# Kernel tuning notes

Measured on AMD Instinct MI355X. Metric: run time of the kernel, lower is better.

Reference implementation:

```python
import jax, jax.numpy as jnp
import numpy as np

B, T, DIM = 2, 1024, 4096
H, Hk, D = 32, 8, 128
NREP = H // Hk
SCALE = 1.0 / np.sqrt(D)
LAMBDA_INIT = 0.8 - 0.6 * np.exp(-0.3 * 0)  # layer_idx=0 -> 0.2
EPS = 1e-6


def setup_inputs() -> dict:
    key = jax.random.key(0)
    ks = jax.random.split(key, 12)
    x = jax.random.normal(ks[0], (B, T, DIM), dtype=jnp.float32)
    cos = jax.random.uniform(ks[1], (T, D // 2), dtype=jnp.float32)
    sin = jax.random.uniform(ks[2], (T, D // 2), dtype=jnp.float32)
    wq = jax.random.normal(ks[3], (DIM, 2 * H * D), dtype=jnp.float32) * 0.02
    wk = jax.random.normal(ks[4], (DIM, 2 * Hk * D), dtype=jnp.float32) * 0.02
    wv = jax.random.normal(ks[5], (DIM, Hk * D), dtype=jnp.float32) * 0.02
    wo = jax.random.normal(ks[6], (H * D, DIM), dtype=jnp.float32) * 0.02
    lambda_q1 = jax.random.normal(ks[7], (H, D), dtype=jnp.float32) * 0.1
    lambda_k1 = jax.random.normal(ks[8], (H, D), dtype=jnp.float32) * 0.1
    lambda_q2 = jax.random.normal(ks[9], (H, D), dtype=jnp.float32) * 0.1
    lambda_k2 = jax.random.normal(ks[10], (H, D), dtype=jnp.float32) * 0.1
    subln_w = jnp.ones((D,), dtype=jnp.float32)
    return {"x": x, "cos": cos, "sin": sin, "wq": wq, "wk": wk, "wv": wv,
            "wo": wo, "lambda_q1": lambda_q1, "lambda_k1": lambda_k1,
            "lambda_q2": lambda_q2, "lambda_k2": lambda_k2, "subln_w": subln_w}


def _rope(xh, cos, sin):
    # xh: [B, h, T, D]; cos/sin: [T, D/2]
    x1, x2 = xh[..., : D // 2], xh[..., D // 2:]
    c = cos[None, None, :, :]
    s = sin[None, None, :, :]
    return jnp.concatenate([x1 * c - x2 * s, x2 * c + x1 * s], axis=-1)


def _causal_attn(q, k, v):
    # q,k,v: [B, H, T, D]
    s = jnp.einsum("bhqd,bhkd->bhqk", q, k) * SCALE
    causal = jnp.tril(jnp.ones((T, T), dtype=bool))
    s = jnp.where(causal[None, None], s, jnp.finfo(s.dtype).min)
    p = jax.nn.softmax(s, axis=-1)
    return jnp.einsum("bhqk,bhkd->bhqd", p, v)


def reference(x, cos, sin, wq, wk, wv, wo, lambda_q1, lambda_k1, lambda_q2, lambda_k2, subln_w):
    q_full = (x @ wq).reshape(B, T, 2 * H, D).transpose(0, 2, 1, 3)   # [B,2H,T,D]
    k_full = (x @ wk).reshape(B, T, 2 * Hk, D).transpose(0, 2, 1, 3)  # [B,2Hk,T,D]
    v = (x @ wv).reshape(B, T, Hk, D).transpose(0, 2, 1, 3)           # [B,Hk,T,D]

    q1, q2 = q_full[:, :H], q_full[:, H:]
    k1, k2 = k_full[:, :Hk], k_full[:, Hk:]

    q1 = _rope(q1, cos, sin)
    q2 = _rope(q2, cos, sin)
    k1 = _rope(k1, cos, sin)
    k2 = _rope(k2, cos, sin)

    def expand_kv(kv):  # [B,Hk,T,D] -> [B,H,T,D] (GQA repeat)
        return jnp.repeat(kv, NREP, axis=1)

    k1e, k2e, ve = expand_kv(k1), expand_kv(k2), expand_kv(v)

    a1 = _causal_attn(q1, k1e, ve)
    a2 = _causal_attn(q2, k2e, ve)

    lam = (jnp.exp(jnp.sum(lambda_q1 * lambda_k1, axis=-1))
           - jnp.exp(jnp.sum(lambda_q2 * lambda_k2, axis=-1))
           + LAMBDA_INIT)  # [H]
    diff = a1 - lam[None, :, None, None] * a2  # [B,H,T,D]

    # per-head-dim RMSNorm (subln)
    rms = jax.lax.rsqrt(jnp.mean(diff * diff, axis=-1, keepdims=True) + EPS)
    diff = diff * rms * subln_w

    out = diff.transpose(0, 2, 1, 3).reshape(B, T, H * D)
    return out @ wo
```

## Files before the change

kernel.cpp:

```cpp
#include <hip/hip_runtime.h>
#include <hip/hip_bf16.h>
#include <stdint.h>

typedef unsigned short u16;
typedef unsigned int u32;
typedef short bf16x8 __attribute__((ext_vector_type(8)));
typedef float f32x4 __attribute__((ext_vector_type(4)));

#define SCALE_F 0.088388347648318447f
#define LAMBDA_INIT_F 0.2f

__device__ __forceinline__ u16 f2bf(float f) {
  union { float f; u32 u; } v; v.f = f;
  u32 r = v.u + 0x7fffu + ((v.u >> 16) & 1u);
  return (u16)(r >> 16);
}
__device__ __forceinline__ float bf2f(u16 u) {
  union { u32 u; float f; } v; v.u = ((u32)u) << 16;
  return v.f;
}

typedef __attribute__((address_space(1))) void gvoid_t;
typedef __attribute__((address_space(3))) void lvoid_t;
__device__ __forceinline__ void gload16(const void* g, void* l) {
  __builtin_amdgcn_global_load_lds((gvoid_t*)g, (lvoid_t*)l, 16, 0, 0);
}

__global__ void cast_f32_bf16(const float4* __restrict__ in, uint2* __restrict__ out, int n4) {
  int i = blockIdx.x * 256 + threadIdx.x;
  if (i >= n4) return;
  float4 v = in[i];
  uint2 o;
  o.x = (u32)f2bf(v.x) | ((u32)f2bf(v.y) << 16);
  o.y = (u32)f2bf(v.z) | ((u32)f2bf(v.w) << 16);
  out[i] = o;
}

__global__ void trans_cast(const float* __restrict__ in, u16* __restrict__ out, int K, int N) {
  __shared__ float tile[64][33];
  int kt = blockIdx.y * 64, nt = blockIdx.x * 32;
  int x = threadIdx.x, y = threadIdx.y;
  #pragma unroll
  for (int j = 0; j < 8; ++j)
    tile[y + j * 8][x] = in[(size_t)(kt + y + j * 8) * N + nt + x];
  __syncthreads();
  #pragma unroll
  for (int j = 0; j < 4; ++j) {
    int n = y * 4 + j;
    u32 pk = (u32)f2bf(tile[2 * x][n]) | ((u32)f2bf(tile[2 * x + 1][n]) << 16);
    *(u32*)&out[(size_t)(nt + n) * K + kt + 2 * x] = pk;
  }
}

#define SQA(buf, t) { \
  gload16(Aq + (size_t)(t) * 32, (buf) + qdst); \
  gload16(Aq + (size_t)64 * K + (size_t)(t) * 32, (buf) + 2048 + qdst); }
#define SQB(buf, t) { \
  gload16(Bq + (size_t)(t) * 32, (buf) + qdst); \
  gload16(Bq + (size_t)64 * K + (size_t)(t) * 32, (buf) + 2048 + qdst); \
  gload16(Bq + (size_t)128 * K + (size_t)(t) * 32, (buf) + 4096 + qdst); \
  gload16(Bq + (size_t)192 * K + (size_t)(t) * 32, (buf) + 6144 + qdst); }
#define QMFMA16(O) { \
  acc[O+0][0] = __builtin_amdgcn_mfma_f32_16x16x32_bf16(a0, b0, acc[O+0][0], 0, 0, 0); \
  acc[O+0][1] = __builtin_amdgcn_mfma_f32_16x16x32_bf16(a0, b1, acc[O+0][1], 0, 0, 0); \
  acc[O+0][2] = __builtin_amdgcn_mfma_f32_16x16x32_bf16(a0, b2, acc[O+0][2], 0, 0, 0); \
  acc[O+0][3] = __builtin_amdgcn_mfma_f32_16x16x32_bf16(a0, b3, acc[O+0][3], 0, 0, 0); \
  acc[O+1][0] = __builtin_amdgcn_mfma_f32_16x16x32_bf16(a1, b0, acc[O+1][0], 0, 0, 0); \
  acc[O+1][1] = __builtin_amdgcn_mfma_f32_16x16x32_bf16(a1, b1, acc[O+1][1], 0, 0, 0); \
  acc[O+1][2] = __builtin_amdgcn_mfma_f32_16x16x32_bf16(a1, b2, acc[O+1][2], 0, 0, 0); \
  acc[O+1][3] = __builtin_amdgcn_mfma_f32_16x16x32_bf16(a1, b3, acc[O+1][3], 0, 0, 0); \
  acc[O+2][0] = __builtin_amdgcn_mfma_f32_16x16x32_bf16(a2, b0, acc[O+2][0], 0, 0, 0); \
  acc[O+2][1] = __builtin_amdgcn_mfma_f32_16x16x32_bf16(a2, b1, acc[O+2][1], 0, 0, 0); \
  acc[O+2][2] = __builtin_amdgcn_mfma_f32_16x16x32_bf16(a2, b2, acc[O+2][2], 0, 0, 0); \
  acc[O+2][3] = __builtin_amdgcn_mfma_f32_16x16x32_bf16(a2, b3, acc[O+2][3], 0, 0, 0); \
  acc[O+3][0] = __builtin_amdgcn_mfma_f32_16x16x32_bf16(a3, b0, acc[O+3][0], 0, 0, 0); \
  acc[O+3][1] = __builtin_amdgcn_mfma_f32_16x16x32_bf16(a3, b1, acc[O+3][1], 0, 0, 0); \
  acc[O+3][2] = __builtin_amdgcn_mfma_f32_16x16x32_bf16(a3, b2, acc[O+3][2], 0, 0, 0); \
  acc[O+3][3] = __builtin_amdgcn_mfma_f32_16x16x32_bf16(a3, b3, acc[O+3][3], 0, 0, 0); }

__global__ __launch_bounds__(256, 2) void gemmW(const u16* __restrict__ A,
                                                const u16* __restrict__ Bt,
                                                u16* __restrict__ C,
                                                int M, int N, int K, int TN) {
  extern __shared__ u16 lds[];
  const int tid = threadIdx.x;
  const int lane = tid & 63;
  const int wn = tid >> 6;
  const int ln = lane & 15, gr = lane >> 4;
  const int NT = K >> 5;

  const int bid = blockIdx.x;
  const int bn = (bid % TN) * 256;
  const int bm = (bid / TN) * 128;

  const int sch = (tid & 3) ^ ((tid >> 3) & 3);
  const u16* Aq = A + (size_t)(bm + (tid >> 2)) * K + sch * 8;
  const u16* Bq = Bt + (size_t)(bn + (tid >> 2)) * K + sch * 8;
  const int qdst = tid * 8;

  const int cfo = (gr ^ ((ln >> 1) & 3)) * 8;
  const int ab = ln * 32 + cfo;
  const int bb = wn * 2048 + ln * 32 + cfo;

  f32x4 acc[8][4] = {};
  bf16x8 a0, a1, a2, a3, b0, b1, b2, b3;

  SQA(lds, 0);
  SQB(lds + 12288, 0);
  SQA(lds + 4096, 1);
  SQB(lds + 20480, 1);
  asm volatile("s_waitcnt vmcnt(6)" ::: "memory");
  __builtin_amdgcn_s_barrier();

  int tm3 = 0;
  for (int t = 0; t < NT; ++t) {
    const u16* Ac = lds + tm3 * 4096;
    const u16* Bc = lds + 12288 + tm3 * 8192;
    int tn3 = tm3 + 2; if (tn3 >= 3) tn3 -= 3;
    u16* An = lds + tn3 * 4096;
    u16* Bn = lds + 12288 + tn3 * 8192;

    a0 = *(const bf16x8*)&Ac[ab];
    a1 = *(const bf16x8*)&Ac[ab + 512];
    a2 = *(const bf16x8*)&Ac[ab + 1024];
    a3 = *(const bf16x8*)&Ac[ab + 1536];
    b0 = *(const bf16x8*)&Bc[bb];
    b1 = *(const bf16x8*)&Bc[bb + 512];
    b2 = *(const bf16x8*)&Bc[bb + 1024];
    b3 = *(const bf16x8*)&Bc[bb + 1536];
    if (t + 2 < NT) SQA(An, t + 2);
    __builtin_amdgcn_s_setprio(1);
    QMFMA16(0);
    __builtin_amdgcn_s_setprio(0);

    a0 = *(const bf16x8*)&Ac[ab + 2048];
    a1 = *(const bf16x8*)&Ac[ab + 2560];
    a2 = *(const bf16x8*)&Ac[ab + 3072];
    a3 = *(const bf16x8*)&Ac[ab + 3584];
    if (t + 2 < NT) {
      SQB(Bn, t + 2);
      asm volatile("s_waitcnt vmcnt(6)" ::: "memory");
    } else {
      asm volatile("s_waitcnt vmcnt(0)" ::: "memory");
    }
    __builtin_amdgcn_s_setprio(1);
    QMFMA16(4);
    __builtin_amdgcn_s_setprio(0);
    __builtin_amdgcn_s_barrier();

    tm3 = (tm3 + 1 == 3) ? 0 : tm3 + 1;
  }

  #pragma unroll
  for (int mf = 0; mf < 8; ++mf) {
    #pragma unroll
    for (int j = 0; j < 4; ++j) {
      int r = bm + mf * 16 + gr * 4 + j;
      #pragma unroll
      for (int nf = 0; nf < 4; ++nf) {
        int c = bn + wn * 64 + nf * 16 + ln;
        C[(size_t)r * N + c] = f2bf(acc[mf][nf][j]);
      }
    }
  }
}

#define STA(buf, t) { \
  gload16(Ab + (size_t)(t) * 64, (buf) + dsloc); \
  gload16(Ab + (size_t)32 * K + (size_t)(t) * 64, (buf) + 2048 + dsloc); \
  gload16(Ab + (size_t)64 * K + (size_t)(t) * 64, (buf) + 4096 + dsloc); \
  gload16(Ab + (size_t)96 * K + (size_t)(t) * 64, (buf) + 6144 + dsloc); }
#define STB(buf, t) { \
  gload16(Bb + (size_t)(t) * 64, (buf) + dsloc); \
  gload16(Bb + (size_t)32 * K + (size_t)(t) * 64, (buf) + 2048 + dsloc); \
  gload16(Bb + (size_t)64 * K + (size_t)(t) * 64, (buf) + 4096 + dsloc); \
  gload16(Bb + (size_t)96 * K + (size_t)(t) * 64, (buf) + 6144 + dsloc); }
#define MFMA16 { \
  acc[0][0] = __builtin_amdgcn_mfma_f32_16x16x32_bf16(a0, b0, acc[0][0], 0, 0, 0); \
  acc[0][1] = __builtin_amdgcn_mfma_f32_16x16x32_bf16(a0, b1, acc[0][1], 0, 0, 0); \
  acc[0][2] = __builtin_amdgcn_mfma_f32_16x16x32_bf16(a0, b2, acc[0][2], 0, 0, 0); \
  acc[0][3] = __builtin_amdgcn_mfma_f32_16x16x32_bf16(a0, b3, acc[0][3], 0, 0, 0); \
  acc[1][0] = __builtin_amdgcn_mfma_f32_16x16x32_bf16(a1, b0, acc[1][0], 0, 0, 0); \
  acc[1][1] = __builtin_amdgcn_mfma_f32_16x16x32_bf16(a1, b1, acc[1][1], 0, 0, 0); \
  acc[1][2] = __builtin_amdgcn_mfma_f32_16x16x32_bf16(a1, b2, acc[1][2], 0, 0, 0); \
  acc[1][3] = __builtin_amdgcn_mfma_f32_16x16x32_bf16(a1, b3, acc[1][3], 0, 0, 0); \
  acc[2][0] = __builtin_amdgcn_mfma_f32_16x16x32_bf16(a2, b0, acc[2][0], 0, 0, 0); \
  acc[2][1] = __builtin_amdgcn_mfma_f32_16x16x32_bf16(a2, b1, acc[2][1], 0, 0, 0); \
  acc[2][2] = __builtin_amdgcn_mfma_f32_16x16x32_bf16(a2, b2, acc[2][2], 0, 0, 0); \
  acc[2][3] = __builtin_amdgcn_mfma_f32_16x16x32_bf16(a2, b3, acc[2][3], 0, 0, 0); \
  acc[3][0] = __builtin_amdgcn_mfma_f32_16x16x32_bf16(a3, b0, acc[3][0], 0, 0, 0); \
  acc[3][1] = __builtin_amdgcn_mfma_f32_16x16x32_bf16(a3, b1, acc[3][1], 0, 0, 0); \
  acc[3][2] = __builtin_amdgcn_mfma_f32_16x16x32_bf16(a3, b2, acc[3][2], 0, 0, 0); \
  acc[3][3] = __builtin_amdgcn_mfma_f32_16x16x32_bf16(a3, b3, acc[3][3], 0, 0, 0); }

template <bool OUT_BF16>
__global__ __launch_bounds__(256, 2) void gemm8p(const u16* __restrict__ A,
                                                 const u16* __restrict__ Bt,
                                                 void* __restrict__ Cv,
                                                 int M, int N, int K, int TN) {
  extern __shared__ u16 lds[];
  const int tid = threadIdx.x;
  const int lane = tid & 63;
  const int wid = tid >> 6;
  const int wm = wid >> 1, wn = wid & 1;
  const int ln = lane & 15, gr = lane >> 4;
  const int NT = K >> 6;

  const int bid = blockIdx.x;
  const int bn = (bid % TN) * 128;
  const int bm = (bid / TN) * 128;

  const int srow = tid >> 3;
  const int sch = (tid & 7) ^ (srow & 7);
  const u16* Ab = A + (size_t)(bm + srow) * K + sch * 8;
  const u16* Bb = Bt + (size_t)(bn + srow) * K + sch * 8;
  const int dsloc = tid * 8;

  const int aro = (wm * 64 + ln) * 64;
  const int bro = (wn * 64 + ln) * 64;
  const int c0 = (gr ^ (ln & 7)) * 8;
  const int c1 = ((4 + gr) ^ (ln & 7)) * 8;

  f32x4 acc[4][4] = {};
  bf16x8 a0, a1, a2, a3, b0, b1, b2, b3;

  STA(lds, 0);
  STB(lds + 16384, 0);
  STB(lds + 24576, 1);
  asm volatile("s_waitcnt vmcnt(4)" ::: "memory");
  __builtin_amdgcn_s_barrier();

  int tm3 = 0;
  for (int t = 0; t < NT; ++t) {
    const u16* Ac = lds + (t & 1) * 8192;
    u16* An = lds + ((t + 1) & 1) * 8192;
    const u16* Bc = lds + 16384 + tm3 * 8192;
    int tn3 = tm3 + 2; if (tn3 >= 3) tn3 -= 3;
    u16* Bn = lds + 16384 + tn3 * 8192;

    a0 = *(const bf16x8*)&Ac[aro + c0];
    a1 = *(const bf16x8*)&Ac[aro + 1024 + c0];
    a2 = *(const bf16x8*)&Ac[aro + 2048 + c0];
    a3 = *(const bf16x8*)&Ac[aro + 3072 + c0];
    b0 = *(const bf16x8*)&Bc[bro + c0];
    b1 = *(const bf16x8*)&Bc[bro + 1024 + c0];
    b2 = *(const bf16x8*)&Bc[bro + 2048 + c0];
    b3 = *(const bf16x8*)&Bc[bro + 3072 + c0];
    if (t + 1 < NT) STA(An, t + 1);
    __builtin_amdgcn_s_setprio(1);
    MFMA16;
    __builtin_amdgcn_s_setprio(0);

    a0 = *(const bf16x8*)&Ac[aro + c1];
    a1 = *(const bf16x8*)&Ac[aro + 1024 + c1];
    a2 = *(const bf16x8*)&Ac[aro + 2048 + c1];
    a3 = *(const bf16x8*)&Ac[aro + 3072 + c1];
    b0 = *(const bf16x8*)&Bc[bro + c1];
    b1 = *(const bf16x8*)&Bc[bro + 1024 + c1];
    b2 = *(const bf16x8*)&Bc[bro + 2048 + c1];
    b3 = *(const bf16x8*)&Bc[bro + 3072 + c1];
    if (t + 2 < NT) {
      STB(Bn, t + 2);
      asm volatile("s_waitcnt vmcnt(4)" ::: "memory");
    } else {
      asm volatile("s_waitcnt vmcnt(0)" ::: "memory");
    }
    __builtin_amdgcn_s_setprio(1);
    MFMA16;
    __builtin_amdgcn_s_setprio(0);
    __builtin_amdgcn_s_barrier();

    tm3 = (tm3 + 1 == 3) ? 0 : tm3 + 1;
  }

  #pragma unroll
  for (int mf = 0; mf < 4; ++mf) {
    #pragma unroll
    for (int j = 0; j < 4; ++j) {
      int r = bm + wm * 64 + mf * 16 + gr * 4 + j;
      #pragma unroll
      for (int nf = 0; nf < 4; ++nf) {
        int c = bn + wn * 64 + nf * 16 + ln;
        if (OUT_BF16) ((u16*)Cv)[(size_t)r * N + c] = f2bf(acc[mf][nf][j]);
        else          ((float*)Cv)[(size_t)r * N + c] = acc[mf][nf][j];
      }
    }
  }
}

__global__ void rope_kernel(const u16* __restrict__ in, u16* __restrict__ out,
                            const float* __restrict__ cosp, const float* __restrict__ sinp,
                            int NHh, int col_off) {
  int idx = blockIdx.x * 256 + threadIdx.x;
  int c = idx & 7;
  int t = (idx >> 3) & 1023;
  int h = (idx >> 13) % NHh;
  int b = (idx >> 13) / NHh;
  size_t src = (size_t)(b * 1024 + t) * 11264 + col_off + h * 128 + c * 8;
  bf16x8 v1 = *(const bf16x8*)&in[src];
  bf16x8 v2 = *(const bf16x8*)&in[src + 64];
  const float4* cp = (const float4*)&cosp[t * 64 + c * 8];
  const float4* sp = (const float4*)&sinp[t * 64 + c * 8];
  float4 c0 = cp[0], c1 = cp[1], s0 = sp[0], s1 = sp[1];
  float cc[8] = {c0.x, c0.y, c0.z, c0.w, c1.x, c1.y, c1.z, c1.w};
  float ss[8] = {s0.x, s0.y, s0.z, s0.w, s1.x, s1.y, s1.z, s1.w};
  bf16x8 o1, o2;
  #pragma unroll
  for (int e = 0; e < 8; ++e) {
    float x1 = bf2f((u16)v1[e]);
    float x2 = bf2f((u16)v2[e]);
    o1[e] = (short)f2bf(x1 * cc[e] - x2 * ss[e]);
    o2[e] = (short)f2bf(x2 * cc[e] + x1 * ss[e]);
  }
  size_t dst = ((size_t)(b * NHh + h) * 1024 + t) * 128 + c * 8;
  *(bf16x8*)&out[dst] = o1;
  *(bf16x8*)&out[dst + 64] = o2;
}

__global__ void vtrans_kernel(const u16* __restrict__ qkv, u16* __restrict__ vt) {
  __shared__ u16 tile[32][34];
  int bh = blockIdx.z;
  int t0 = blockIdx.x * 32, d0 = blockIdx.y * 32;
  int b = bh >> 3, hk = bh & 7;
  int x = threadIdx.x, y = threadIdx.y;
  #pragma unroll
  for (int j = 0; j < 32; j += 8)
    tile[y + j][x] = qkv[(size_t)(b * 1024 + t0 + y + j) * 11264 + 10240 + hk * 128 + d0 + x];
  __syncthreads();
  #pragma unroll
  for (int j = 0; j < 32; j += 8)
    vt[((size_t)bh * 128 + d0 + y + j) * 1024 + t0 + x] = tile[x][y + j];
}

__global__ void lam_kernel(const float* __restrict__ lq1, const float* __restrict__ lk1,
                           const float* __restrict__ lq2, const float* __restrict__ lk2,
                           float* __restrict__ lam) {
  int h = blockIdx.x, l = threadIdx.x;
  float p1 = lq1[h * 128 + l] * lk1[h * 128 + l] + lq1[h * 128 + 64 + l] * lk1[h * 128 + 64 + l];
  float p2 = lq2[h * 128 + l] * lk2[h * 128 + l] + lq2[h * 128 + 64 + l] * lk2[h * 128 + 64 + l];
  #pragma unroll
  for (int m = 32; m >= 1; m >>= 1) { p1 += __shfl_xor(p1, m); p2 += __shfl_xor(p2, m); }
  if (l == 0) lam[h] = expf(p1) - expf(p2) + LAMBDA_INIT_F;
}

__global__ __launch_bounds__(512) void attn_kernel(const u16* __restrict__ qr,
                                                   const u16* __restrict__ kr,
                                                   const u16* __restrict__ vt,
                                                   const float* __restrict__ lam,
                                                   const float* __restrict__ slw,
                                                   u16* __restrict__ attno) {
  __shared__ u16 k1s[2][32 * 136];
  __shared__ u16 k2s[2][32 * 136];
  __shared__ u16 vs[2][128 * 40];
  __shared__ u16 ps[8][2][640];
  const int bx = blockIdx.x, h = blockIdx.y, b = blockIdx.z;
  const int qt = (b == 0) ? (7 - bx) : bx;
  const int tid = threadIdx.x, lane = tid & 63, w = tid >> 6;
  const int ln = lane & 15, gr = lane >> 4;
  const int hk = h >> 2;
  const int qrow0 = qt * 128 + w * 16;
  u16* psw1 = ps[w][0];
  u16* psw2 = ps[w][1];
  const float SL2E = 0.12751744006165926f;
  const float ML2E = 11.541560327111707f;

  bf16x8 q1f[4], q2f[4];
  {
    const u16* q1p = qr + ((size_t)(b * 64 + h) * 1024 + qrow0 + ln) * 128 + gr * 8;
    const u16* q2p = qr + ((size_t)(b * 64 + 32 + h) * 1024 + qrow0 + ln) * 128 + gr * 8;
    #pragma unroll
    for (int ds = 0; ds < 4; ++ds) {
      q1f[ds] = *(const bf16x8*)(q1p + ds * 32);
      q2f[ds] = *(const bf16x8*)(q2p + ds * 32);
    }
  }
  f32x4 acc1[8] = {}, acc2[8] = {};
  float l1[4] = {0.f, 0.f, 0.f, 0.f}, l2[4] = {0.f, 0.f, 0.f, 0.f};

  const u16* k1g = kr + (size_t)(b * 16 + hk) * 1024 * 128;
  const u16* k2g = kr + (size_t)(b * 16 + 8 + hk) * 1024 * 128;
  const u16* vg = vt + (size_t)(b * 8 + hk) * 128 * 1024;
  const int nkt = 4 * qt + 4;

  const int krow = tid >> 4, kch = tid & 15;
  const int vdr = tid >> 2, vch = tid & 3;
  const u16* k1p = k1g + (size_t)krow * 128 + kch * 8;
  const u16* k2p = k2g + (size_t)krow * 128 + kch * 8;
  const u16* vp = vg + (size_t)vdr * 1024 + vch * 8;
  const int kdst = krow * 136 + kch * 8;
  const int vdst = vdr * 40 + vch * 8;

  bf16x8 r0 = *(const bf16x8*)(k1p);
  bf16x8 r1 = *(const bf16x8*)(k2p);
  bf16x8 r2 = *(const bf16x8*)(vp);
  *(bf16x8*)&k1s[0][kdst] = r0;
  *(bf16x8*)&k2s[0][kdst] = r1;
  *(bf16x8*)&vs[0][vdst] = r2;
  __syncthreads();

  int cur = 0;
  for (int kt = 0; kt < nkt; ++kt) {
    if (kt + 1 < nkt) {
      r0 = *(const bf16x8*)(k1p + (size_t)(kt + 1) * 4096);
      r1 = *(const bf16x8*)(k2p + (size_t)(kt + 1) * 4096);
      r2 = *(const bf16x8*)(vp + (size_t)(kt + 1) * 32);
    }

    f32x4 s1[2], s2[2];
    #pragma unroll
    for (int ct = 0; ct < 2; ++ct) {
      s1[ct] = (f32x4){0.f, 0.f, 0.f, 0.f};
      s2[ct] = (f32x4){0.f, 0.f, 0.f, 0.f};
      #pragma unroll
      for (int ds = 0; ds < 4; ++ds) {
        bf16x8 kf1 = *(const bf16x8*)&k1s[cur][(ct * 16 + ln) * 136 + ds * 32 + gr * 8];
        s1[ct] = __builtin_amdgcn_mfma_f32_16x16x32_bf16(q1f[ds], kf1, s1[ct], 0, 0, 0);
        bf16x8 kf2 = *(const bf16x8*)&k2s[cur][(ct * 16 + ln) * 136 + ds * 32 + gr * 8];
        s2[ct] = __builtin_amdgcn_mfma_f32_16x16x32_bf16(q2f[ds], kf2, s2[ct], 0, 0, 0);
      }
    }
    #pragma unroll
    for (int j = 0; j < 4; ++j) {
      int row = qrow0 + gr * 4 + j;
      bool msk0 = (kt * 32 + ln) > row;
      bool msk1 = (kt * 32 + 16 + ln) > row;
      float t10 = msk0 ? -1e30f : fmaf(s1[0][j], SL2E, -ML2E);
      float t11 = msk1 ? -1e30f : fmaf(s1[1][j], SL2E, -ML2E);
      float t20 = msk0 ? -1e30f : fmaf(s2[0][j], SL2E, -ML2E);
      float t21 = msk1 ? -1e30f : fmaf(s2[1][j], SL2E, -ML2E);
      u16 b10 = f2bf(exp2f(t10)), b11 = f2bf(exp2f(t11));
      u16 b20 = f2bf(exp2f(t20)), b21 = f2bf(exp2f(t21));
      int ro = (gr * 4 + j) * 40;
      psw1[ro + ln] = b10; psw1[ro + 16 + ln] = b11;
      psw2[ro + ln] = b20; psw2[ro + 16 + ln] = b21;
      l1[j] += bf2f(b10) + bf2f(b11);
      l2[j] += bf2f(b20) + bf2f(b21);
    }
    bf16x8 pf1 = *(const bf16x8*)&psw1[ln * 40 + gr * 8];
    bf16x8 pf2 = *(const bf16x8*)&psw2[ln * 40 + gr * 8];
    #pragma unroll
    for (int dt = 0; dt < 8; ++dt) {
      bf16x8 vf = *(const bf16x8*)&vs[cur][(dt * 16 + ln) * 40 + gr * 8];
      acc1[dt] = __builtin_amdgcn_mfma_f32_16x16x32_bf16(pf1, vf, acc1[dt], 0, 0, 0);
      acc2[dt] = __builtin_amdgcn_mfma_f32_16x16x32_bf16(pf2, vf, acc2[dt], 0, 0, 0);
    }

    if (kt + 1 < nkt) {
      *(bf16x8*)&k1s[cur ^ 1][kdst] = r0;
      *(bf16x8*)&k2s[cur ^ 1][kdst] = r1;
      *(bf16x8*)&vs[cur ^ 1][vdst] = r2;
    }
    __syncthreads();
    cur ^= 1;
  }

  float inv1[4], inv2[4];
  #pragma unroll
  for (int j = 0; j < 4; ++j) {
    float a = l1[j], c = l2[j];
    a += __shfl_xor(a, 1); a += __shfl_xor(a, 2); a += __shfl_xor(a, 4); a += __shfl_xor(a, 8);
    c += __shfl_xor(c, 1); c += __shfl_xor(c, 2); c += __shfl_xor(c, 4); c += __shfl_xor(c, 8);
    inv1[j] = 1.f / a;
    inv2[j] = 1.f / c;
  }

  float lamv = lam[h];
  float ssq[4] = {0.f, 0.f, 0.f, 0.f};
  #pragma unroll
  for (int dt = 0; dt < 8; ++dt)
    #pragma unroll
    for (int j = 0; j < 4; ++j) {
      float d = acc1[dt][j] * inv1[j] - lamv * (acc2[dt][j] * inv2[j]);
      acc1[dt][j] = d;
      ssq[j] += d * d;
    }
  #pragma unroll
  for (int j = 0; j < 4; ++j) {
    float s = ssq[j];
    s += __shfl_xor(s, 1);
    s += __shfl_xor(s, 2);
    s += __shfl_xor(s, 4);
    s += __shfl_xor(s, 8);
    ssq[j] = rsqrtf(s * (1.0f / 128.0f) + 1e-6f);
  }
  #pragma unroll
  for (int dt = 0; dt < 8; ++dt) {
    float wgt = slw[dt * 16 + ln];
    #pragma unroll
    for (int j = 0; j < 4; ++j) {
      int row = qrow0 + gr * 4 + j;
      attno[(size_t)(b * 1024 + row) * 4096 + h * 128 + dt * 16 + ln] = f2bf(acc1[dt][j] * ssq[j] * wgt);
    }
  }
}

extern "C" void kernel_launch(void* const* d_in, const int* in_sizes, int n_in,
                              void* d_out, int out_size, void* d_ws, size_t ws_size,
                              hipStream_t stream) {
  (void)in_sizes; (void)n_in; (void)out_size; (void)ws_size;
  const float* x    = (const float*)d_in[0];
  const float* cosp = (const float*)d_in[1];
  const float* sinp = (const float*)d_in[2];
  const float* wq   = (const float*)d_in[3];
  const float* wk   = (const float*)d_in[4];
  const float* wv   = (const float*)d_in[5];
  const float* wo   = (const float*)d_in[6];
  const float* lq1  = (const float*)d_in[7];
  const float* lk1  = (const float*)d_in[8];
  const float* lq2  = (const float*)d_in[9];
  const float* lk2  = (const float*)d_in[10];
  const float* slw  = (const float*)d_in[11];
  float* out = (float*)d_out;
  char* ws = (char*)d_ws;

  u16* xb    = (u16*)(ws);
  u16* wqkvt = (u16*)(ws + 16777216);
  u16* qr    = (u16*)(ws + 16777216);
  u16* kr    = (u16*)(ws + 50331648);
  u16* vtp   = (u16*)(ws + 58720256);
  u16* attno = (u16*)(ws + 62914560);
  u16* qkv   = (u16*)(ws + 109051904);
  u16* wot   = (u16*)(ws + 109051904);
  float* lam = (float*)(ws + 155189248);

  cast_f32_bf16<<<8192, 256, 0, stream>>>((const float4*)x, (uint2*)xb, 2097152);
  trans_cast<<<dim3(256, 64), dim3(32, 8), 0, stream>>>(wq, wqkvt, 4096, 8192);
  trans_cast<<<dim3(64, 64),  dim3(32, 8), 0, stream>>>(wk, wqkvt + (size_t)8192 * 4096, 4096, 2048);
  trans_cast<<<dim3(32, 64),  dim3(32, 8), 0, stream>>>(wv, wqkvt + (size_t)10240 * 4096, 4096, 1024);
  gemmW<<<704, 256, 73728, stream>>>(xb, wqkvt, qkv, 2048, 11264, 4096, 44);
  rope_kernel<<<4096, 256, 0, stream>>>(qkv, qr, cosp, sinp, 64, 0);
  rope_kernel<<<1024, 256, 0, stream>>>(qkv, kr, cosp, sinp, 16, 8192);
  vtrans_kernel<<<dim3(32, 4, 16), dim3(32, 8), 0, stream>>>(qkv, vtp);
  trans_cast<<<dim3(128, 64), dim3(32, 8), 0, stream>>>(wo, wot, 4096, 4096);
  lam_kernel<<<32, 64, 0, stream>>>(lq1, lk1, lq2, lk2, lam);
  attn_kernel<<<dim3(8, 32, 2), 512, 0, stream>>>(qr, kr, vtp, lam, slw, attno);
  gemm8p<false><<<512, 256, 81920, stream>>>(attno, wot, (void*)out, 2048, 4096, 4096, 32);
}
```

Measured before the change: 431.3 us.

## Fuse RoPE and head-major scatter into QKV GEMM epilogue

The QKV projection GEMM now stages its output tile in LDS and applies RoPE directly in the epilogue, writing rotated Q and K in head-major layout. V columns go to a compact buffer. This removes the two standalone rope kernels and the round trip of the full QKV intermediate through global memory. In exchange the GEMM epilogue gains an extra LDS pass, a barrier and more complex scattered writes, and the workspace layout is reshuffled.

Result: faster. 419.5 us, median of 2 (-2.8%).

```diff
diff --git a/kernel.cpp b/kernel.cpp
--- a/kernel.cpp
+++ b/kernel.cpp
@@ -80,8 +80,12 @@
 
 __global__ __launch_bounds__(256, 2) void gemmW(const u16* __restrict__ A,
                                                 const u16* __restrict__ Bt,
-                                                u16* __restrict__ C,
-                                                int M, int N, int K, int TN) {
+                                                u16* __restrict__ vb,
+                                                u16* __restrict__ qrp,
+                                                u16* __restrict__ krp,
+                                                const float* __restrict__ cosp,
+                                                const float* __restrict__ sinp,
+                                                int K, int TN) {
   extern __shared__ u16 lds[];
   const int tid = threadIdx.x;
   const int lane = tid & 63;
@@ -151,17 +155,56 @@
     tm3 = (tm3 + 1 == 3) ? 0 : tm3 + 1;
   }
 
-  #pragma unroll
-  for (int mf = 0; mf < 8; ++mf) {
-    #pragma unroll
-    for (int j = 0; j < 4; ++j) {
-      int r = bm + mf * 16 + gr * 4 + j;
+  if (bn < 10240) {
+    #pragma unroll
+    for (int mf = 0; mf < 8; ++mf)
       #pragma unroll
-      for (int nf = 0; nf < 4; ++nf) {
-        int c = bn + wn * 64 + nf * 16 + ln;
-        C[(size_t)r * N + c] = f2bf(acc[mf][nf][j]);
+      for (int j = 0; j < 4; ++j) {
+        int rl = mf * 16 + gr * 4 + j;
+        #pragma unroll
+        for (int nf = 0; nf < 4; ++nf)
+          lds[rl * 264 + wn * 64 + nf * 16 + ln] = f2bf(acc[mf][nf][j]);
       }
-    }
+    __syncthreads();
+    const int bb_ = bm >> 10;
+    const int gt0 = bm & 1023;
+    const bool isQ = (bn < 8192);
+    const int hbase = isQ ? (bn >> 7) : ((bn - 8192) >> 7);
+    const int NHh = isQ ? 64 : 16;
+    u16* outp = isQ ? qrp : krp;
+    const int tr = tid >> 5;
+    const int d2 = (tid & 31) * 2;
+    #pragma unroll
+    for (int r8 = 0; r8 < 16; ++r8) {
+      int t = r8 * 8 + tr;
+      int gt = gt0 + t;
+      float2 cc = *(const float2*)&cosp[gt * 64 + d2];
+      float2 sv = *(const float2*)&sinp[gt * 64 + d2];
+      #pragma unroll
+      for (int hh = 0; hh < 2; ++hh) {
+        u32 p1 = *(const u32*)&lds[t * 264 + hh * 128 + d2];
+        u32 p2 = *(const u32*)&lds[t * 264 + hh * 128 + 64 + d2];
+        float x1a = bf2f((u16)p1), x1b = bf2f((u16)(p1 >> 16));
+        float x2a = bf2f((u16)p2), x2b = bf2f((u16)(p2 >> 16));
+        u32 o1 = (u32)f2bf(x1a * cc.x - x2a * sv.x) | ((u32)f2bf(x1b * cc.y - x2b * sv.y) << 16);
+        u32 o2 = (u32)f2bf(x2a * cc.x + x1a * sv.x) | ((u32)f2bf(x2b * cc.y + x1b * sv.y) << 16);
+        size_t base = ((size_t)(bb_ * NHh + hbase + hh) * 1024 + gt) * 128;
+        *(u32*)&outp[base + d2] = o1;
+        *(u32*)&outp[base + 64 + d2] = o2;
+      }
+    }
+  } else {
+    #pragma unroll
+    for (int mf = 0; mf < 8; ++mf)
+      #pragma unroll
+      for (int j = 0; j < 4; ++j) {
+        int r = bm + mf * 16 + gr * 4 + j;
+        #pragma unroll
+        for (int nf = 0; nf < 4; ++nf) {
+          int vc = bn - 10240 + wn * 64 + nf * 16 + ln;
+          vb[(size_t)r * 1024 + vc] = f2bf(acc[mf][nf][j]);
+        }
+      }
   }
 }
 
@@ -288,36 +331,7 @@
   }
 }
 
-__global__ void rope_kernel(const u16* __restrict__ in, u16* __restrict__ out,
-                            const float* __restrict__ cosp, const float* __restrict__ sinp,
-                            int NHh, int col_off) {
-  int idx = blockIdx.x * 256 + threadIdx.x;
-  int c = idx & 7;
-  int t = (idx >> 3) & 1023;
-  int h = (idx >> 13) % NHh;
-  int b = (idx >> 13) / NHh;
-  size_t src = (size_t)(b * 1024 + t) * 11264 + col_off + h * 128 + c * 8;
-  bf16x8 v1 = *(const bf16x8*)&in[src];
-  bf16x8 v2 = *(const bf16x8*)&in[src + 64];
-  const float4* cp = (const float4*)&cosp[t * 64 + c * 8];
-  const float4* sp = (const float4*)&sinp[t * 64 + c * 8];
-  float4 c0 = cp[0], c1 = cp[1], s0 = sp[0], s1 = sp[1];
-  float cc[8] = {c0.x, c0.y, c0.z, c0.w, c1.x, c1.y, c1.z, c1.w};
-  float ss[8] = {s0.x, s0.y, s0.z, s0.w, s1.x, s1.y, s1.z, s1.w};
-  bf16x8 o1, o2;
-  #pragma unroll
-  for (int e = 0; e < 8; ++e) {
-    float x1 = bf2f((u16)v1[e]);
-    float x2 = bf2f((u16)v2[e]);
-    o1[e] = (short)f2bf(x1 * cc[e] - x2 * ss[e]);
-    o2[e] = (short)f2bf(x2 * cc[e] + x1 * ss[e]);
-  }
-  size_t dst = ((size_t)(b * NHh + h) * 1024 + t) * 128 + c * 8;
-  *(bf16x8*)&out[dst] = o1;
-  *(bf16x8*)&out[dst + 64] = o2;
-}
-
-__global__ void vtrans_kernel(const u16* __restrict__ qkv, u16* __restrict__ vt) {
+__global__ void vtrans_kernel(const u16* __restrict__ vb, u16* __restrict__ vt) {
   __shared__ u16 tile[32][34];
   int bh = blockIdx.z;
   int t0 = blockIdx.x * 32, d0 = blockIdx.y * 32;
@@ -325,7 +339,7 @@
   int x = threadIdx.x, y = threadIdx.y;
   #pragma unroll
   for (int j = 0; j < 32; j += 8)
-    tile[y + j][x] = qkv[(size_t)(b * 1024 + t0 + y + j) * 11264 + 10240 + hk * 128 + d0 + x];
+    tile[y + j][x] = vb[(size_t)(b * 1024 + t0 + y + j) * 1024 + hk * 128 + d0 + x];
   __syncthreads();
   #pragma unroll
   for (int j = 0; j < 32; j += 8)
@@ -514,23 +528,21 @@
   char* ws = (char*)d_ws;
 
   u16* xb    = (u16*)(ws);
+  u16* vtp   = (u16*)(ws);
   u16* wqkvt = (u16*)(ws + 16777216);
-  u16* qr    = (u16*)(ws + 16777216);
-  u16* kr    = (u16*)(ws + 50331648);
-  u16* vtp   = (u16*)(ws + 58720256);
-  u16* attno = (u16*)(ws + 62914560);
-  u16* qkv   = (u16*)(ws + 109051904);
-  u16* wot   = (u16*)(ws + 109051904);
+  u16* wot   = (u16*)(ws + 16777216);
+  u16* attno = (u16*)(ws + 50331648);
+  u16* qr    = (u16*)(ws + 109051904);
+  u16* kr    = (u16*)(ws + 142606336);
+  u16* vbuf  = (u16*)(ws + 150994944);
   float* lam = (float*)(ws + 155189248);
 
   cast_f32_bf16<<<8192, 256, 0, stream>>>((const float4*)x, (uint2*)xb, 2097152);
   trans_cast<<<dim3(256, 64), dim3(32, 8), 0, stream>>>(wq, wqkvt, 4096, 8192);
   trans_cast<<<dim3(64, 64),  dim3(32, 8), 0, stream>>>(wk, wqkvt + (size_t)8192 * 4096, 4096, 2048);
   trans_cast<<<dim3(32, 64),  dim3(32, 8), 0, stream>>>(wv, wqkvt + (size_t)10240 * 4096, 4096, 1024);
-  gemmW<<<704, 256, 73728, stream>>>(xb, wqkvt, qkv, 2048, 11264, 4096, 44);
-  rope_kernel<<<4096, 256, 0, stream>>>(qkv, qr, cosp, sinp, 64, 0);
-  rope_kernel<<<1024, 256, 0, stream>>>(qkv, kr, cosp, sinp, 16, 8192);
-  vtrans_kernel<<<dim3(32, 4, 16), dim3(32, 8), 0, stream>>>(qkv, vtp);
+  gemmW<<<704, 256, 73728, stream>>>(xb, wqkvt, vbuf, qr, kr, cosp, sinp, 4096, 44);
+  vtrans_kernel<<<dim3(32, 4, 16), dim3(32, 8), 0, stream>>>(vbuf, vtp);
   trans_cast<<<dim3(128, 64), dim3(32, 8), 0, stream>>>(wo, wot, 4096, 4096);
   lam_kernel<<<32, 64, 0, stream>>>(lq1, lk1, lq2, lk2, lam);
   attn_kernel<<<dim3(8, 32, 2), 512, 0, stream>>>(qr, kr, vtp, lam, slw, attno);
```
